# Kernel tuning notes

Hardware: AMD Instinct MI355X
Metric: run time of the kernel (lower is better)

The kernel has to match this reference:

```python
import jax, jax.numpy as jnp
import numpy as np

B, R, NM, H, P1, G1, RC1, LAT = 16384, 360, 200, 256, 512, 256, 256, 128


def _linear_params(k, out_f, in_f):
    s = 1.0 / np.sqrt(in_f)
    kw, kb = jax.random.split(k)
    W = jax.random.uniform(kw, (out_f, in_f), minval=-s, maxval=s, dtype=jnp.float32)
    b = jax.random.uniform(kb, (out_f,), minval=-s, maxval=s, dtype=jnp.float32)
    return W, b


def setup_inputs() -> dict:
    key = jax.random.key(0)
    ks = jax.random.split(key, 14)
    x_window = jax.random.normal(ks[0], (B, 3, R), dtype=jnp.float32)
    modes = jax.random.normal(ks[1], (R, NM), dtype=jnp.float32)
    mode_coeff = jax.random.normal(ks[2], (B, NM), dtype=jnp.float32)
    W1, b1 = _linear_params(ks[3], H, 3 * R)      # surrogate layer 1
    W2, b2 = _linear_params(ks[4], H, H)          # surrogate layer 2
    W3, b3 = _linear_params(ks[5], R, H)          # surrogate layer 3
    Wp1, bp1 = _linear_params(ks[6], P1, R * R)   # npi_proj
    Wp2, bp2 = _linear_params(ks[7], LAT, P1)
    Wg1, bg1 = _linear_params(ks[8], G1, NM)      # geo_proj
    Wg2, bg2 = _linear_params(ks[9], LAT, G1)
    Wr1, br1 = _linear_params(ks[10], RC1, LAT)   # recon
    Wr2, br2 = _linear_params(ks[11], R, RC1)
    return dict(x_window=x_window, modes=modes, mode_coeff=mode_coeff,
                W1=W1, b1=b1, W2=W2, b2=b2, W3=W3, b3=b3,
                Wp1=Wp1, bp1=bp1, Wp2=Wp2, bp2=bp2,
                Wg1=Wg1, bg1=bg1, Wg2=Wg2, bg2=bg2,
                Wr1=Wr1, br1=br1, Wr2=Wr2, br2=br2)


def reference(x_window, modes, mode_coeff,
              W1, b1, W2, b2, W3, b3,
              Wp1, bp1, Wp2, bp2,
              Wg1, bg1, Wg2, bg2,
              Wr1, br1, Wr2, br2):
    Bs = x_window.shape[0]
    Rr = W3.shape[0]
    # ---- NPI surrogate forward (needed for ReLU masks) ----
    z = x_window.reshape(Bs, 3 * Rr)                       # (B, 3R)
    h1 = z @ W1.T + b1                                     # (B, H)
    m1 = (h1 > 0).astype(z.dtype)
    h2 = (h1 * m1) @ W2.T + b2                             # (B, H)
    m2 = (h2 > 0).astype(z.dtype)
    # ---- EC: exact batch-mean Jacobian of the ReLU MLP w.r.t last timestep ----
    # mean_b [ W3 diag(m2_b) W2 diag(m1_b) W1_last ] = W3 @ (W2 * (m2^T m1 / B)) @ W1[:, -R:]
    G = (m2.T @ m1) / Bs                                   # (H, H)
    ec = W3 @ ((W2 * G) @ W1[:, -Rr:])                     # (R, R); row j = dy_j/dx
    ec = jax.lax.stop_gradient(ec)                         # create_graph=False in original
    # ---- projections ----
    ec_flat = ec.reshape(1, Rr * Rr)
    z_npi1 = jax.nn.relu(ec_flat @ Wp1.T + bp1) @ Wp2.T + bp2   # (1, LAT)
    z_npi = jnp.tile(z_npi1, (Bs, 1))                           # (B, LAT)
    z_geo = jax.nn.relu(mode_coeff @ Wg1.T + bg1) @ Wg2.T + bg2  # (B, LAT)
    zsum = z_npi + z_geo
    zn = zsum / jnp.maximum(jnp.linalg.norm(zsum, axis=-1, keepdims=True), 1e-12)
    recon = jax.nn.relu(zn @ Wr1.T + br1) @ Wr2.T + br2          # (B, R)
    return (z_npi, z_geo, zn, ec, recon)
```

## Files before the change

### kernel.cpp

```cpp
#include <hip/hip_runtime.h>

typedef __bf16 bf16x8 __attribute__((ext_vector_type(8)));
typedef __bf16 bf16x4 __attribute__((ext_vector_type(4)));
typedef float  f32x4  __attribute__((ext_vector_type(4)));

__device__ __forceinline__ f32x4 mfma_bf16(bf16x8 a, bf16x8 b, f32x4 c) {
  return __builtin_amdgcn_mfma_f32_16x16x32_bf16(a, b, c, 0, 0, 0);
}
__device__ __forceinline__ bf16x8 ldB(const __bf16* Bp, int kt, int NT, int nt,
                                      int lane) {
  return *reinterpret_cast<const bf16x8*>(Bp + (((size_t)kt * NT + nt) * 64 + lane) * 8);
}

__global__ void pack_all(const float* __restrict__ W1, const float* __restrict__ W2,
                         const float* __restrict__ Wg1, const float* __restrict__ Wg2,
                         const float* __restrict__ Wr1, const float* __restrict__ Wr2,
                         __bf16* __restrict__ W1p, __bf16* __restrict__ W2p,
                         __bf16* __restrict__ Wg1p, __bf16* __restrict__ Wg2p,
                         __bf16* __restrict__ Wr1p, __bf16* __restrict__ Wr2p) {
  int bx = blockIdx.x;
  const float* W; __bf16* out; int N, K, NT, local;
  if (bx < 544)      { W = W1;  out = W1p;  N = 256; K = 1080; NT = 16; local = bx; }
  else if (bx < 672) { W = W2;  out = W2p;  N = 256; K = 256;  NT = 16; local = bx - 544; }
  else if (bx < 784) { W = Wg1; out = Wg1p; N = 256; K = 200;  NT = 16; local = bx - 672; }
  else if (bx < 848) { W = Wg2; out = Wg2p; N = 128; K = 256;  NT = 8;  local = bx - 784; }
  else if (bx < 912) { W = Wr1; out = Wr1p; N = 256; K = 128;  NT = 16; local = bx - 848; }
  else               { W = Wr2; out = Wr2p; N = 360; K = 256;  NT = 24; local = bx - 912; }
  int nt = local % NT, kt = local / NT;
  int lane = threadIdx.x;
  int n = nt * 16 + (lane & 15);
  int k0 = kt * 32 + (lane >> 4) * 8;
  bf16x8 v;
#pragma unroll
  for (int e = 0; e < 8; ++e) {
    int k = k0 + e;
    float xv = (n < N && k < K) ? W[(size_t)n * K + k] : 0.f;
    v[e] = (__bf16)xv;
  }
  *reinterpret_cast<bf16x8*>(out + ((size_t)local * 64 + lane) * 8) = v;
}

__global__ __launch_bounds__(256) void h1h2_fused(
    const float* __restrict__ x, const __bf16* __restrict__ W1p,
    const float* __restrict__ b1, const __bf16* __restrict__ W2p,
    const float* __restrict__ b2, __bf16* __restrict__ m1b,
    __bf16* __restrict__ m2b) {
  __shared__ __bf16 Alds[32][40];
  __shared__ __bf16 h1s[32][264];
  int tid = threadIdx.x;
  int lane = tid & 63, wid = tid >> 6;
  int rowBase = blockIdx.x * 32;
  int sr = tid >> 3, sc = (tid & 7) * 4;
  const float* aSrc = x + (size_t)(rowBase + sr) * 1080;
  f32x4 acc[2][4] = {};
  float4 ld0 = *(const float4*)(aSrc + sc);
  float4 ld1 = *(const float4*)(aSrc + 32 + sc);
  for (int kt = 0; kt < 34; ++kt) {
    bf16x4 w4;
    w4[0] = (__bf16)ld0.x; w4[1] = (__bf16)ld0.y;
    w4[2] = (__bf16)ld0.z; w4[3] = (__bf16)ld0.w;
    *reinterpret_cast<bf16x4*>(&Alds[sr][sc]) = w4;
    __syncthreads();
    ld0 = ld1;
    if (kt + 2 < 34) {
      int gk = (kt + 2) * 32 + sc;
      ld1 = (gk < 1080) ? *(const float4*)(aSrc + gk) : make_float4(0.f, 0.f, 0.f, 0.f);
    }
    int arow = lane & 15, ak = (lane >> 4) * 8;
    bf16x8 a0 = *reinterpret_cast<const bf16x8*>(&Alds[arow][ak]);
    bf16x8 a1 = *reinterpret_cast<const bf16x8*>(&Alds[arow + 16][ak]);
#pragma unroll
    for (int n = 0; n < 4; ++n) {
      bf16x8 bv = ldB(W1p, kt, 16, wid * 4 + n, lane);
      acc[0][n] = mfma_bf16(a0, bv, acc[0][n]);
      acc[1][n] = mfma_bf16(a1, bv, acc[1][n]);
    }
    __syncthreads();
  }
  int q4 = (lane >> 4) * 4;
#pragma unroll
  for (int m = 0; m < 2; ++m)
#pragma unroll
    for (int n = 0; n < 4; ++n) {
      int col = wid * 64 + n * 16 + (lane & 15);
      float bb = b1[col];
#pragma unroll
      for (int j = 0; j < 4; ++j) {
        int rl = m * 16 + q4 + j;
        float h = acc[m][n][j] + bb;
        m1b[(size_t)(rowBase + rl) * 256 + col] = (__bf16)(h > 0.f ? 1.f : 0.f);
        h1s[rl][col] = (__bf16)fmaxf(h, 0.f);
      }
    }
  __syncthreads();
  f32x4 acc2[2][4] = {};
#pragma unroll
  for (int ks = 0; ks < 8; ++ks) {
    int arow = lane & 15, ak = ks * 32 + (lane >> 4) * 8;
    bf16x8 a0 = *reinterpret_cast<const bf16x8*>(&h1s[arow][ak]);
    bf16x8 a1 = *reinterpret_cast<const bf16x8*>(&h1s[arow + 16][ak]);
#pragma unroll
    for (int n = 0; n < 4; ++n) {
      bf16x8 bv = ldB(W2p, ks, 16, wid * 4 + n, lane);
      acc2[0][n] = mfma_bf16(a0, bv, acc2[0][n]);
      acc2[1][n] = mfma_bf16(a1, bv, acc2[1][n]);
    }
  }
#pragma unroll
  for (int m = 0; m < 2; ++m)
#pragma unroll
    for (int n = 0; n < 4; ++n) {
      int col = wid * 64 + n * 16 + (lane & 15);
      float bb = b2[col];
#pragma unroll
      for (int j = 0; j < 4; ++j) {
        int rl = m * 16 + q4 + j;
        float h = acc2[m][n][j] + bb;
        m2b[(size_t)(rowBase + rl) * 256 + col] = (__bf16)(h > 0.f ? 1.f : 0.f);
      }
    }
}

__global__ __launch_bounds__(256) void gemm_masks(
    const __bf16* __restrict__ m2, const __bf16* __restrict__ m1,
    float* __restrict__ Gpart) {
  __shared__ __bf16 Aft[64][40];
  __shared__ __bf16 Bft[64][40];
  int tid = threadIdx.x;
  int lane = tid & 63, wid = tid >> 6;
  int wr = wid >> 1, wc = wid & 1;
  int ibase = blockIdx.x * 64, jbase = blockIdx.y * 64;
  int b0 = blockIdx.z * 1024;
  int skk = tid >> 3, si0 = (tid & 7) * 8;
  f32x4 acc[2][2] = {};
  for (int c = 0; c < 32; ++c) {
    int bb = b0 + c * 32 + skk;
    bf16x8 va = *reinterpret_cast<const bf16x8*>(m2 + (size_t)bb * 256 + ibase + si0);
    bf16x8 vb = *reinterpret_cast<const bf16x8*>(m1 + (size_t)bb * 256 + jbase + si0);
#pragma unroll
    for (int e = 0; e < 8; ++e) {
      int r = si0 + e;
      int cc = skk ^ (((r >> 3) & 3) << 3);
      Aft[r][cc] = va[e];
      Bft[r][cc] = vb[e];
    }
    __syncthreads();
    int ar = wr * 32 + (lane & 15);
    int br = wc * 32 + (lane & 15);
    int k8 = (lane >> 4) * 8;
    bf16x8 a0 = *reinterpret_cast<const bf16x8*>(&Aft[ar][k8 ^ (((ar >> 3) & 3) << 3)]);
    bf16x8 a1 = *reinterpret_cast<const bf16x8*>(
        &Aft[ar + 16][k8 ^ ((((ar + 16) >> 3) & 3) << 3)]);
    bf16x8 bv0 = *reinterpret_cast<const bf16x8*>(&Bft[br][k8 ^ (((br >> 3) & 3) << 3)]);
    bf16x8 bv1 = *reinterpret_cast<const bf16x8*>(
        &Bft[br + 16][k8 ^ ((((br + 16) >> 3) & 3) << 3)]);
    acc[0][0] = mfma_bf16(a0, bv0, acc[0][0]);
    acc[0][1] = mfma_bf16(a0, bv1, acc[0][1]);
    acc[1][0] = mfma_bf16(a1, bv0, acc[1][0]);
    acc[1][1] = mfma_bf16(a1, bv1, acc[1][1]);
    __syncthreads();
  }
  float* dst = Gpart + (size_t)blockIdx.z * 65536;
  int q4 = (lane >> 4) * 4;
#pragma unroll
  for (int m = 0; m < 2; ++m)
#pragma unroll
    for (int n = 0; n < 2; ++n)
#pragma unroll
      for (int j = 0; j < 4; ++j) {
        int gi = ibase + wr * 32 + m * 16 + q4 + j;
        int gj = jbase + wc * 32 + n * 16 + (lane & 15);
        dst[(size_t)gi * 256 + gj] = acc[m][n][j];
      }
}

__global__ void reduce_G(const float* __restrict__ Gpart, float* __restrict__ G) {
  int i = blockIdx.x * 256 + threadIdx.x;
  float s = 0.f;
#pragma unroll
  for (int z = 0; z < 16; ++z) s += Gpart[(size_t)z * 65536 + i];
  G[i] = s * (1.f / 16384.f);
}

__global__ __launch_bounds__(256) void small_gemm(
    const float* __restrict__ A, const float* __restrict__ A2, int lda,
    const float* __restrict__ Bm, int ldb, float* __restrict__ C, int ldc,
    int M, int N, int K) {
  __shared__ float As[64][17];
  __shared__ float Bs[16][65];
  int t = threadIdx.x;
  int tx = t & 15, ty = t >> 4;
  int m0 = blockIdx.y * 64, n0 = blockIdx.x * 64;
  float acc[4][4] = {};
  for (int k0 = 0; k0 < K; k0 += 16) {
#pragma unroll
    for (int i = 0; i < 4; ++i) {
      int idx = t * 4 + i;
      int r = idx >> 4, kk = idx & 15;
      int gm = m0 + r, gk = k0 + kk;
      float v = (gm < M && gk < K) ? A[(size_t)gm * lda + gk] : 0.f;
      if (A2 && gm < M && gk < K) v *= A2[(size_t)gm * lda + gk];
      As[r][kk] = v;
      int kk2 = idx >> 6, cc = idx & 63;
      int gk2 = k0 + kk2, gn = n0 + cc;
      Bs[kk2][cc] = (gk2 < K && gn < N) ? Bm[(size_t)gk2 * ldb + gn] : 0.f;
    }
    __syncthreads();
#pragma unroll
    for (int kk = 0; kk < 16; ++kk)
#pragma unroll
      for (int i = 0; i < 4; ++i)
#pragma unroll
        for (int j = 0; j < 4; ++j)
          acc[i][j] += As[ty * 4 + i][kk] * Bs[kk][tx * 4 + j];
    __syncthreads();
  }
#pragma unroll
  for (int i = 0; i < 4; ++i)
#pragma unroll
    for (int j = 0; j < 4; ++j) {
      int gm = m0 + ty * 4 + i, gn = n0 + tx * 4 + j;
      if (gm < M && gn < N) C[(size_t)gm * ldc + gn] = acc[i][j];
    }
}

__global__ __launch_bounds__(512) void p_and_g1(
    const float* __restrict__ Wp1, const float* __restrict__ ec,
    const float* __restrict__ bp1, float* __restrict__ p,
    const float* __restrict__ mc, const __bf16* __restrict__ Wg1p,
    const float* __restrict__ bg1, __bf16* __restrict__ g1b) {
  __shared__ __bf16 Alds[64][40];
  __shared__ float redw[8];
  int t = threadIdx.x;
  if (blockIdx.x < 512) {
    int row = blockIdx.x;
    const float4* w = (const float4*)(Wp1 + (size_t)row * 129600);
    const float4* e = (const float4*)ec;
    float s = 0.f;
    for (int i = t; i < 32400; i += 512) {
      float4 a = w[i], b = e[i];
      s += a.x * b.x + a.y * b.y + a.z * b.z + a.w * b.w;
    }
    for (int o = 32; o; o >>= 1) s += __shfl_down(s, o);
    if ((t & 63) == 0) redw[t >> 6] = s;
    __syncthreads();
    if (t == 0) {
      float tot = 0.f;
#pragma unroll
      for (int i = 0; i < 8; ++i) tot += redw[i];
      p[row] = fmaxf(tot + bp1[row], 0.f);
    }
  } else {
    int lane = t & 63, wid = t >> 6;
    int wr = wid >> 2, wc = wid & 3;
    int rowBase = (blockIdx.x - 512) * 64;
    int sr = t >> 3, sc = (t & 7) * 4;
    const float* aSrc = mc + (size_t)(rowBase + sr) * 200;
    f32x4 acc[2][4] = {};
    for (int kt = 0; kt < 7; ++kt) {
      int gk = kt * 32 + sc;
      bf16x4 w4;
      if (gk < 200) {
        float4 v = *(const float4*)(aSrc + gk);
        w4[0] = (__bf16)v.x; w4[1] = (__bf16)v.y;
        w4[2] = (__bf16)v.z; w4[3] = (__bf16)v.w;
      } else {
        w4[0] = w4[1] = w4[2] = w4[3] = (__bf16)0.f;
      }
      *reinterpret_cast<bf16x4*>(&Alds[sr][sc]) = w4;
      __syncthreads();
      int arow = wr * 32 + (lane & 15), ak = (lane >> 4) * 8;
      bf16x8 a0 = *reinterpret_cast<const bf16x8*>(&Alds[arow][ak]);
      bf16x8 a1 = *reinterpret_cast<const bf16x8*>(&Alds[arow + 16][ak]);
#pragma unroll
      for (int n = 0; n < 4; ++n) {
        bf16x8 bv = ldB(Wg1p, kt, 16, wc * 4 + n, lane);
        acc[0][n] = mfma_bf16(a0, bv, acc[0][n]);
        acc[1][n] = mfma_bf16(a1, bv, acc[1][n]);
      }
      __syncthreads();
    }
    int q4 = (lane >> 4) * 4;
#pragma unroll
    for (int m = 0; m < 2; ++m)
#pragma unroll
      for (int n = 0; n < 4; ++n) {
        int col = wc * 64 + n * 16 + (lane & 15);
        float bb = bg1[col];
#pragma unroll
        for (int j = 0; j < 4; ++j) {
          int rl = wr * 32 + m * 16 + q4 + j;
          g1b[(size_t)(rowBase + rl) * 256 + col] =
              (__bf16)fmaxf(acc[m][n][j] + bb, 0.f);
        }
      }
  }
}

__global__ void gemv_z(const float* __restrict__ p, const float* __restrict__ Wp2,
                       const float* __restrict__ bp2, float* __restrict__ znpi1) {
  __shared__ float pl[512];
  int t = threadIdx.x;
  pl[t] = p[t];
  pl[t + 256] = p[t + 256];
  __syncthreads();
  if (t < 128) {
    float s = bp2[t];
    const float* w = Wp2 + (size_t)t * 512;
    for (int k = 0; k < 512; ++k) s += pl[k] * w[k];
    znpi1[t] = s;
  }
}

__global__ __launch_bounds__(512) void mega_tail(
    const __bf16* __restrict__ g1b, const __bf16* __restrict__ Wg2p,
    const float* __restrict__ bg2, const float* __restrict__ znpi1,
    const __bf16* __restrict__ Wr1p, const float* __restrict__ br1,
    const __bf16* __restrict__ Wr2p, const float* __restrict__ br2,
    float* __restrict__ o_zgeo, float* __restrict__ o_znpi,
    float* __restrict__ o_zn, float* __restrict__ o_rec) {
  __shared__ __align__(16) char smem[64 * 264 * 2 + 64 * 136 * 2];
  __bf16 (*Abig)[264] = (__bf16(*)[264])smem;
  __bf16 (*r1S)[264] = (__bf16(*)[264])smem;
  __bf16 (*znS)[136] = (__bf16(*)[136])(smem + 64 * 264 * 2);
  __shared__ float red[4][64];
  int tid = threadIdx.x;
  int lane = tid & 63, wid = tid >> 6;
  int wr = wid >> 2, wc = wid & 3;
  int rowBase = blockIdx.x * 64;
  int q4 = (lane >> 4) * 4;
  {
    int r = tid >> 3, c0 = (tid & 7) * 32;
    const __bf16* src = g1b + (size_t)(rowBase + r) * 256 + c0;
#pragma unroll
    for (int i = 0; i < 4; ++i)
      *reinterpret_cast<bf16x8*>(&Abig[r][c0 + i * 8]) =
          *reinterpret_cast<const bf16x8*>(src + i * 8);
  }
  __syncthreads();
  float zs[2][2][4];
  {
    f32x4 acc[2][2] = {};
#pragma unroll
    for (int ks = 0; ks < 8; ++ks) {
      int arow = wr * 32 + (lane & 15), ak = ks * 32 + (lane >> 4) * 8;
      bf16x8 a0 = *reinterpret_cast<const bf16x8*>(&Abig[arow][ak]);
      bf16x8 a1 = *reinterpret_cast<const bf16x8*>(&Abig[arow + 16][ak]);
#pragma unroll
      for (int n = 0; n < 2; ++n) {
        bf16x8 bv = ldB(Wg2p, ks, 8, wc * 2 + n, lane);
        acc[0][n] = mfma_bf16(a0, bv, acc[0][n]);
        acc[1][n] = mfma_bf16(a1, bv, acc[1][n]);
      }
    }
#pragma unroll
    for (int m = 0; m < 2; ++m)
#pragma unroll
      for (int n = 0; n < 2; ++n) {
        int col = wc * 32 + n * 16 + (lane & 15);
        float bb = bg2[col], zv = znpi1[col];
#pragma unroll
        for (int j = 0; j < 4; ++j) {
          int row = rowBase + wr * 32 + m * 16 + q4 + j;
          float zg = acc[m][n][j] + bb;
          o_zgeo[(size_t)row * 128 + col] = zg;
          o_znpi[(size_t)row * 128 + col] = zv;
          zs[m][n][j] = zg + zv;
        }
      }
#pragma unroll
    for (int m = 0; m < 2; ++m)
#pragma unroll
      for (int j = 0; j < 4; ++j) {
        float pp = zs[m][0][j] * zs[m][0][j] + zs[m][1][j] * zs[m][1][j];
        pp += __shfl_xor(pp, 1);
        pp += __shfl_xor(pp, 2);
        pp += __shfl_xor(pp, 4);
        pp += __shfl_xor(pp, 8);
        if ((lane & 15) == 0) red[wc][wr * 32 + m * 16 + q4 + j] = pp;
      }
    __syncthreads();
#pragma unroll
    for (int m = 0; m < 2; ++m)
#pragma unroll
      for (int n = 0; n < 2; ++n) {
        int col = wc * 32 + n * 16 + (lane & 15);
#pragma unroll
        for (int j = 0; j < 4; ++j) {
          int rl = wr * 32 + m * 16 + q4 + j;
          float ss = red[0][rl] + red[1][rl] + red[2][rl] + red[3][rl];
          float rn = 1.f / fmaxf(sqrtf(ss), 1e-12f);
          float z = zs[m][n][j] * rn;
          o_zn[(size_t)(rowBase + rl) * 128 + col] = z;
          znS[rl][col] = (__bf16)z;
        }
      }
  }
  __syncthreads();
  {
    f32x4 acc[2][4] = {};
#pragma unroll
    for (int ks = 0; ks < 4; ++ks) {
      int arow = wr * 32 + (lane & 15), ak = ks * 32 + (lane >> 4) * 8;
      bf16x8 a0 = *reinterpret_cast<const bf16x8*>(&znS[arow][ak]);
      bf16x8 a1 = *reinterpret_cast<const bf16x8*>(&znS[arow + 16][ak]);
#pragma unroll
      for (int n = 0; n < 4; ++n) {
        bf16x8 bv = ldB(Wr1p, ks, 16, wc * 4 + n, lane);
        acc[0][n] = mfma_bf16(a0, bv, acc[0][n]);
        acc[1][n] = mfma_bf16(a1, bv, acc[1][n]);
      }
    }
#pragma unroll
    for (int m = 0; m < 2; ++m)
#pragma unroll
      for (int n = 0; n < 4; ++n) {
        int col = wc * 64 + n * 16 + (lane & 15);
        float bb = br1[col];
#pragma unroll
        for (int j = 0; j < 4; ++j) {
          int rl = wr * 32 + m * 16 + q4 + j;
          r1S[rl][col] = (__bf16)fmaxf(acc[m][n][j] + bb, 0.f);
        }
      }
  }
  __syncthreads();
  {
    f32x4 acc[2][6] = {};
#pragma unroll
    for (int ks = 0; ks < 8; ++ks) {
      int arow = wr * 32 + (lane & 15), ak = ks * 32 + (lane >> 4) * 8;
      bf16x8 a0 = *reinterpret_cast<const bf16x8*>(&r1S[arow][ak]);
      bf16x8 a1 = *reinterpret_cast<const bf16x8*>(&r1S[arow + 16][ak]);
#pragma unroll
      for (int n = 0; n < 6; ++n) {
        bf16x8 bv = ldB(Wr2p, ks, 24, wc * 6 + n, lane);
        acc[0][n] = mfma_bf16(a0, bv, acc[0][n]);
        acc[1][n] = mfma_bf16(a1, bv, acc[1][n]);
      }
    }
#pragma unroll
    for (int m = 0; m < 2; ++m)
#pragma unroll
      for (int n = 0; n < 6; ++n) {
        int col = wc * 96 + n * 16 + (lane & 15);
        if (col < 360) {
          float bb = br2[col];
#pragma unroll
          for (int j = 0; j < 4; ++j) {
            int rl = wr * 32 + m * 16 + q4 + j;
            o_rec[(size_t)(rowBase + rl) * 360 + col] = acc[m][n][j] + bb;
          }
        }
      }
  }
}

extern "C" void kernel_launch(void* const* d_in, const int* in_sizes, int n_in,
                              void* d_out, int out_size, void* d_ws,
                              size_t ws_size, hipStream_t stream) {
  (void)in_sizes; (void)n_in; (void)out_size; (void)ws_size;
  const float* x   = (const float*)d_in[0];
  const float* mc  = (const float*)d_in[2];
  const float* W1  = (const float*)d_in[3];  const float* b1  = (const float*)d_in[4];
  const float* W2  = (const float*)d_in[5];  const float* b2  = (const float*)d_in[6];
  const float* W3  = (const float*)d_in[7];
  const float* Wp1 = (const float*)d_in[9];  const float* bp1 = (const float*)d_in[10];
  const float* Wp2 = (const float*)d_in[11]; const float* bp2 = (const float*)d_in[12];
  const float* Wg1 = (const float*)d_in[13]; const float* bg1 = (const float*)d_in[14];
  const float* Wg2 = (const float*)d_in[15]; const float* bg2 = (const float*)d_in[16];
  const float* Wr1 = (const float*)d_in[17]; const float* br1 = (const float*)d_in[18];
  const float* Wr2 = (const float*)d_in[19]; const float* br2 = (const float*)d_in[20];

  float* out = (float*)d_out;
  float* o_znpi = out;
  float* o_zgeo = out + 2097152;
  float* o_zn   = out + 4194304;
  float* o_ec   = out + 6291456;
  float* o_rec  = out + 6421056;

  char* ws = (char*)d_ws;
  __bf16* m1b   = (__bf16*)(ws + 0);
  __bf16* m2b   = (__bf16*)(ws + 8388608);
  __bf16* g1b   = (__bf16*)(ws + 16777216);
  float*  Gpart = (float*)(ws + 25165824);
  float*  G     = (float*)(ws + 29360128);
  float*  T     = (float*)(ws + 29622272);
  float*  p512  = (float*)(ws + 30015488);
  float*  znpi1 = (float*)(ws + 30017536);
  __bf16* W1p   = (__bf16*)(ws + 30018048);
  __bf16* W2p   = W1p  + (size_t)544 * 512;
  __bf16* Wg1p  = W2p  + (size_t)128 * 512;
  __bf16* Wg2p  = Wg1p + (size_t)112 * 512;
  __bf16* Wr1p  = Wg2p + (size_t)64 * 512;
  __bf16* Wr2p  = Wr1p + (size_t)64 * 512;

  pack_all<<<1104, 64, 0, stream>>>(W1, W2, Wg1, Wg2, Wr1, Wr2,
                                    W1p, W2p, Wg1p, Wg2p, Wr1p, Wr2p);
  h1h2_fused<<<512, 256, 0, stream>>>(x, W1p, b1, W2p, b2, m1b, m2b);
  gemm_masks<<<dim3(4, 4, 16), 256, 0, stream>>>(m2b, m1b, Gpart);
  reduce_G<<<256, 256, 0, stream>>>(Gpart, G);
  small_gemm<<<dim3(6, 4), 256, 0, stream>>>(W2, G, 256, W1 + 720, 1080, T, 384,
                                             256, 360, 256);
  small_gemm<<<dim3(6, 6), 256, 0, stream>>>(W3, nullptr, 256, T, 384, o_ec, 360,
                                             360, 360, 256);
  p_and_g1<<<768, 512, 0, stream>>>(Wp1, o_ec, bp1, p512, mc, Wg1p, bg1, g1b);
  gemv_z<<<1, 256, 0, stream>>>(p512, Wp2, bp2, znpi1);
  mega_tail<<<256, 512, 0, stream>>>(g1b, Wg2p, bg2, znpi1, Wr1p, br1, Wr2p, br2,
                                     o_zgeo, o_znpi, o_zn, o_rec);
}
```

Measured before the change: 261.8 us.

## Transpose mask layout, fuse G reduction via atomics, move geo layer 2 upstream

Writes the ReLU masks batch-transposed so the mask Gram GEMM reads MFMA operands straight from global memory without an LDS transpose or barriers. It accumulates G with atomics, zeroing it inside the pack kernel, which removes the partial buffer and the reduce kernel. It also fuses the second geo projection into p_and_g1 so the g1 intermediate never goes to memory, parallelizes the GEMV across 128 blocks, and doubles the K step in the first GEMM. The cost is float atomic contention, nondeterministic summation order, strided transposed mask stores, and extra LDS in p_and_g1 that may lower occupancy.

Result: faster. 245.9 us, median of 2 (-6.1%).

```diff
diff --git a/kernel.cpp b/kernel.cpp
--- a/kernel.cpp
+++ b/kernel.cpp
@@ -17,8 +17,17 @@
                          const float* __restrict__ Wr1, const float* __restrict__ Wr2,
                          __bf16* __restrict__ W1p, __bf16* __restrict__ W2p,
                          __bf16* __restrict__ Wg1p, __bf16* __restrict__ Wg2p,
-                         __bf16* __restrict__ Wr1p, __bf16* __restrict__ Wr2p) {
+                         __bf16* __restrict__ Wr1p, __bf16* __restrict__ Wr2p,
+                         float* __restrict__ G) {
   int bx = blockIdx.x;
+  int lane = threadIdx.x;
+  if (bx >= 1104) {
+    float4* g = (float4*)G;
+    int base = (bx - 1104) * 512 + lane;
+#pragma unroll
+    for (int i = 0; i < 8; ++i) g[base + i * 64] = make_float4(0.f, 0.f, 0.f, 0.f);
+    return;
+  }
   const float* W; __bf16* out; int N, K, NT, local;
   if (bx < 544)      { W = W1;  out = W1p;  N = 256; K = 1080; NT = 16; local = bx; }
   else if (bx < 672) { W = W2;  out = W2p;  N = 256; K = 256;  NT = 16; local = bx - 544; }
@@ -27,7 +36,6 @@
   else if (bx < 912) { W = Wr1; out = Wr1p; N = 256; K = 128;  NT = 16; local = bx - 848; }
   else               { W = Wr2; out = Wr2p; N = 360; K = 256;  NT = 24; local = bx - 912; }
   int nt = local % NT, kt = local / NT;
-  int lane = threadIdx.x;
   int n = nt * 16 + (lane & 15);
   int k0 = kt * 32 + (lane >> 4) * 8;
   bf16x8 v;
@@ -43,37 +51,50 @@
 __global__ __launch_bounds__(256) void h1h2_fused(
     const float* __restrict__ x, const __bf16* __restrict__ W1p,
     const float* __restrict__ b1, const __bf16* __restrict__ W2p,
-    const float* __restrict__ b2, __bf16* __restrict__ m1b,
-    __bf16* __restrict__ m2b) {
-  __shared__ __bf16 Alds[32][40];
+    const float* __restrict__ b2, __bf16* __restrict__ m1T,
+    __bf16* __restrict__ m2T) {
+  __shared__ __bf16 Alds[32][68];
   __shared__ __bf16 h1s[32][264];
   int tid = threadIdx.x;
   int lane = tid & 63, wid = tid >> 6;
   int rowBase = blockIdx.x * 32;
-  int sr = tid >> 3, sc = (tid & 7) * 4;
+  int sr = tid >> 3, sc = (tid & 7) * 8;
   const float* aSrc = x + (size_t)(rowBase + sr) * 1080;
   f32x4 acc[2][4] = {};
-  float4 ld0 = *(const float4*)(aSrc + sc);
-  float4 ld1 = *(const float4*)(aSrc + 32 + sc);
-  for (int kt = 0; kt < 34; ++kt) {
-    bf16x4 w4;
-    w4[0] = (__bf16)ld0.x; w4[1] = (__bf16)ld0.y;
-    w4[2] = (__bf16)ld0.z; w4[3] = (__bf16)ld0.w;
-    *reinterpret_cast<bf16x4*>(&Alds[sr][sc]) = w4;
-    __syncthreads();
-    ld0 = ld1;
-    if (kt + 2 < 34) {
-      int gk = (kt + 2) * 32 + sc;
-      ld1 = (gk < 1080) ? *(const float4*)(aSrc + gk) : make_float4(0.f, 0.f, 0.f, 0.f);
-    }
-    int arow = lane & 15, ak = (lane >> 4) * 8;
-    bf16x8 a0 = *reinterpret_cast<const bf16x8*>(&Alds[arow][ak]);
-    bf16x8 a1 = *reinterpret_cast<const bf16x8*>(&Alds[arow + 16][ak]);
-#pragma unroll
-    for (int n = 0; n < 4; ++n) {
-      bf16x8 bv = ldB(W1p, kt, 16, wid * 4 + n, lane);
-      acc[0][n] = mfma_bf16(a0, bv, acc[0][n]);
-      acc[1][n] = mfma_bf16(a1, bv, acc[1][n]);
+  float4 c0a, c0b, c1a, c1b;
+  auto LD = [&](int s, float4& a, float4& b) {
+    int gk = s * 64 + sc;
+    if (gk < 1080) {
+      a = *(const float4*)(aSrc + gk);
+      b = *(const float4*)(aSrc + gk + 4);
+    } else {
+      a = make_float4(0.f, 0.f, 0.f, 0.f);
+      b = a;
+    }
+  };
+  LD(0, c0a, c0b);
+  LD(1, c1a, c1b);
+  for (int s = 0; s < 17; ++s) {
+    bf16x8 w8;
+    w8[0] = (__bf16)c0a.x; w8[1] = (__bf16)c0a.y; w8[2] = (__bf16)c0a.z; w8[3] = (__bf16)c0a.w;
+    w8[4] = (__bf16)c0b.x; w8[5] = (__bf16)c0b.y; w8[6] = (__bf16)c0b.z; w8[7] = (__bf16)c0b.w;
+    *reinterpret_cast<bf16x8*>(&Alds[sr][sc]) = w8;
+    __syncthreads();
+    c0a = c1a; c0b = c1b;
+    if (s + 2 < 17) LD(s + 2, c1a, c1b);
+    int arow = lane & 15;
+#pragma unroll
+    for (int ks = 0; ks < 2; ++ks) {
+      int ak = ks * 32 + (lane >> 4) * 8;
+      bf16x8 a0 = *reinterpret_cast<const bf16x8*>(&Alds[arow][ak]);
+      bf16x8 a1 = *reinterpret_cast<const bf16x8*>(&Alds[arow + 16][ak]);
+      int kt = s * 2 + ks;
+#pragma unroll
+      for (int n = 0; n < 4; ++n) {
+        bf16x8 bv = ldB(W1p, kt, 16, wid * 4 + n, lane);
+        acc[0][n] = mfma_bf16(a0, bv, acc[0][n]);
+        acc[1][n] = mfma_bf16(a1, bv, acc[1][n]);
+      }
     }
     __syncthreads();
   }
@@ -88,7 +109,7 @@
       for (int j = 0; j < 4; ++j) {
         int rl = m * 16 + q4 + j;
         float h = acc[m][n][j] + bb;
-        m1b[(size_t)(rowBase + rl) * 256 + col] = (__bf16)(h > 0.f ? 1.f : 0.f);
+        m1T[(size_t)col * 16384 + rowBase + rl] = (__bf16)(h > 0.f ? 1.f : 0.f);
         h1s[rl][col] = (__bf16)fmaxf(h, 0.f);
       }
     }
@@ -116,51 +137,35 @@
       for (int j = 0; j < 4; ++j) {
         int rl = m * 16 + q4 + j;
         float h = acc2[m][n][j] + bb;
-        m2b[(size_t)(rowBase + rl) * 256 + col] = (__bf16)(h > 0.f ? 1.f : 0.f);
+        m2T[(size_t)col * 16384 + rowBase + rl] = (__bf16)(h > 0.f ? 1.f : 0.f);
       }
     }
 }
 
 __global__ __launch_bounds__(256) void gemm_masks(
-    const __bf16* __restrict__ m2, const __bf16* __restrict__ m1,
-    float* __restrict__ Gpart) {
-  __shared__ __bf16 Aft[64][40];
-  __shared__ __bf16 Bft[64][40];
+    const __bf16* __restrict__ m2T, const __bf16* __restrict__ m1T,
+    float* __restrict__ G) {
   int tid = threadIdx.x;
   int lane = tid & 63, wid = tid >> 6;
   int wr = wid >> 1, wc = wid & 1;
   int ibase = blockIdx.x * 64, jbase = blockIdx.y * 64;
-  int b0 = blockIdx.z * 1024;
-  int skk = tid >> 3, si0 = (tid & 7) * 8;
+  size_t b0 = (size_t)blockIdx.z * 1024 + (lane >> 4) * 8;
+  const __bf16* pa0 = m2T + (size_t)(ibase + wr * 32 + (lane & 15)) * 16384 + b0;
+  const __bf16* pa1 = pa0 + (size_t)16 * 16384;
+  const __bf16* pb0 = m1T + (size_t)(jbase + wc * 32 + (lane & 15)) * 16384 + b0;
+  const __bf16* pb1 = pb0 + (size_t)16 * 16384;
   f32x4 acc[2][2] = {};
+#pragma unroll 4
   for (int c = 0; c < 32; ++c) {
-    int bb = b0 + c * 32 + skk;
-    bf16x8 va = *reinterpret_cast<const bf16x8*>(m2 + (size_t)bb * 256 + ibase + si0);
-    bf16x8 vb = *reinterpret_cast<const bf16x8*>(m1 + (size_t)bb * 256 + jbase + si0);
-#pragma unroll
-    for (int e = 0; e < 8; ++e) {
-      int r = si0 + e;
-      int cc = skk ^ (((r >> 3) & 3) << 3);
-      Aft[r][cc] = va[e];
-      Bft[r][cc] = vb[e];
-    }
-    __syncthreads();
-    int ar = wr * 32 + (lane & 15);
-    int br = wc * 32 + (lane & 15);
-    int k8 = (lane >> 4) * 8;
-    bf16x8 a0 = *reinterpret_cast<const bf16x8*>(&Aft[ar][k8 ^ (((ar >> 3) & 3) << 3)]);
-    bf16x8 a1 = *reinterpret_cast<const bf16x8*>(
-        &Aft[ar + 16][k8 ^ ((((ar + 16) >> 3) & 3) << 3)]);
-    bf16x8 bv0 = *reinterpret_cast<const bf16x8*>(&Bft[br][k8 ^ (((br >> 3) & 3) << 3)]);
-    bf16x8 bv1 = *reinterpret_cast<const bf16x8*>(
-        &Bft[br + 16][k8 ^ ((((br + 16) >> 3) & 3) << 3)]);
+    bf16x8 a0 = *reinterpret_cast<const bf16x8*>(pa0 + c * 32);
+    bf16x8 a1 = *reinterpret_cast<const bf16x8*>(pa1 + c * 32);
+    bf16x8 bv0 = *reinterpret_cast<const bf16x8*>(pb0 + c * 32);
+    bf16x8 bv1 = *reinterpret_cast<const bf16x8*>(pb1 + c * 32);
     acc[0][0] = mfma_bf16(a0, bv0, acc[0][0]);
     acc[0][1] = mfma_bf16(a0, bv1, acc[0][1]);
     acc[1][0] = mfma_bf16(a1, bv0, acc[1][0]);
     acc[1][1] = mfma_bf16(a1, bv1, acc[1][1]);
-    __syncthreads();
-  }
-  float* dst = Gpart + (size_t)blockIdx.z * 65536;
+  }
   int q4 = (lane >> 4) * 4;
 #pragma unroll
   for (int m = 0; m < 2; ++m)
@@ -170,16 +175,8 @@
       for (int j = 0; j < 4; ++j) {
         int gi = ibase + wr * 32 + m * 16 + q4 + j;
         int gj = jbase + wc * 32 + n * 16 + (lane & 15);
-        dst[(size_t)gi * 256 + gj] = acc[m][n][j];
-      }
-}
-
-__global__ void reduce_G(const float* __restrict__ Gpart, float* __restrict__ G) {
-  int i = blockIdx.x * 256 + threadIdx.x;
-  float s = 0.f;
-#pragma unroll
-  for (int z = 0; z < 16; ++z) s += Gpart[(size_t)z * 65536 + i];
-  G[i] = s * (1.f / 16384.f);
+        atomicAdd(&G[(size_t)gi * 256 + gj], acc[m][n][j] * (1.f / 16384.f));
+      }
 }
 
 __global__ __launch_bounds__(256) void small_gemm(
@@ -228,8 +225,10 @@
     const float* __restrict__ Wp1, const float* __restrict__ ec,
     const float* __restrict__ bp1, float* __restrict__ p,
     const float* __restrict__ mc, const __bf16* __restrict__ Wg1p,
-    const float* __restrict__ bg1, __bf16* __restrict__ g1b) {
+    const float* __restrict__ bg1, const __bf16* __restrict__ Wg2p,
+    const float* __restrict__ bg2, float* __restrict__ o_zgeo) {
   __shared__ __bf16 Alds[64][40];
+  __shared__ __bf16 g1S[64][264];
   __shared__ float redw[8];
   int t = threadIdx.x;
   if (blockIdx.x < 512) {
@@ -256,6 +255,7 @@
     int rowBase = (blockIdx.x - 512) * 64;
     int sr = t >> 3, sc = (t & 7) * 4;
     const float* aSrc = mc + (size_t)(rowBase + sr) * 200;
+    int q4 = (lane >> 4) * 4;
     f32x4 acc[2][4] = {};
     for (int kt = 0; kt < 7; ++kt) {
       int gk = kt * 32 + sc;
@@ -280,7 +280,6 @@
       }
       __syncthreads();
     }
-    int q4 = (lane >> 4) * 4;
 #pragma unroll
     for (int m = 0; m < 2; ++m)
 #pragma unroll
@@ -290,8 +289,33 @@
 #pragma unroll
         for (int j = 0; j < 4; ++j) {
           int rl = wr * 32 + m * 16 + q4 + j;
-          g1b[(size_t)(rowBase + rl) * 256 + col] =
-              (__bf16)fmaxf(acc[m][n][j] + bb, 0.f);
+          g1S[rl][col] = (__bf16)fmaxf(acc[m][n][j] + bb, 0.f);
+        }
+      }
+    __syncthreads();
+    f32x4 acc2[2][2] = {};
+#pragma unroll
+    for (int ks = 0; ks < 8; ++ks) {
+      int arow = wr * 32 + (lane & 15), ak = ks * 32 + (lane >> 4) * 8;
+      bf16x8 a0 = *reinterpret_cast<const bf16x8*>(&g1S[arow][ak]);
+      bf16x8 a1 = *reinterpret_cast<const bf16x8*>(&g1S[arow + 16][ak]);
+#pragma unroll
+      for (int n = 0; n < 2; ++n) {
+        bf16x8 bv = ldB(Wg2p, ks, 8, wc * 2 + n, lane);
+        acc2[0][n] = mfma_bf16(a0, bv, acc2[0][n]);
+        acc2[1][n] = mfma_bf16(a1, bv, acc2[1][n]);
+      }
+    }
+#pragma unroll
+    for (int m = 0; m < 2; ++m)
+#pragma unroll
+      for (int n = 0; n < 2; ++n) {
+        int col = wc * 32 + n * 16 + (lane & 15);
+        float bb = bg2[col];
+#pragma unroll
+        for (int j = 0; j < 4; ++j) {
+          int row = rowBase + wr * 32 + m * 16 + q4 + j;
+          o_zgeo[(size_t)row * 128 + col] = acc2[m][n][j] + bb;
         }
       }
   }
@@ -299,102 +323,59 @@
 
 __global__ void gemv_z(const float* __restrict__ p, const float* __restrict__ Wp2,
                        const float* __restrict__ bp2, float* __restrict__ znpi1) {
-  __shared__ float pl[512];
+  int j = blockIdx.x;
   int t = threadIdx.x;
-  pl[t] = p[t];
-  pl[t + 256] = p[t + 256];
-  __syncthreads();
-  if (t < 128) {
-    float s = bp2[t];
-    const float* w = Wp2 + (size_t)t * 512;
-    for (int k = 0; k < 512; ++k) s += pl[k] * w[k];
-    znpi1[t] = s;
-  }
+  const float4* w = (const float4*)(Wp2 + (size_t)j * 512);
+  const float4* pp = (const float4*)p;
+  float4 a0 = w[t], b0 = pp[t];
+  float4 a1 = w[t + 64], b1 = pp[t + 64];
+  float s = a0.x * b0.x + a0.y * b0.y + a0.z * b0.z + a0.w * b0.w +
+            a1.x * b1.x + a1.y * b1.y + a1.z * b1.z + a1.w * b1.w;
+  for (int o = 32; o; o >>= 1) s += __shfl_down(s, o);
+  if (t == 0) znpi1[j] = s + bp2[j];
 }
 
 __global__ __launch_bounds__(512) void mega_tail(
-    const __bf16* __restrict__ g1b, const __bf16* __restrict__ Wg2p,
-    const float* __restrict__ bg2, const float* __restrict__ znpi1,
+    const float* __restrict__ zgeo, const float* __restrict__ znpi1,
     const __bf16* __restrict__ Wr1p, const float* __restrict__ br1,
     const __bf16* __restrict__ Wr2p, const float* __restrict__ br2,
-    float* __restrict__ o_zgeo, float* __restrict__ o_znpi,
-    float* __restrict__ o_zn, float* __restrict__ o_rec) {
-  __shared__ __align__(16) char smem[64 * 264 * 2 + 64 * 136 * 2];
-  __bf16 (*Abig)[264] = (__bf16(*)[264])smem;
-  __bf16 (*r1S)[264] = (__bf16(*)[264])smem;
-  __bf16 (*znS)[136] = (__bf16(*)[136])(smem + 64 * 264 * 2);
-  __shared__ float red[4][64];
+    float* __restrict__ o_znpi, float* __restrict__ o_zn,
+    float* __restrict__ o_rec) {
+  __shared__ __bf16 r1S[64][264];
+  __shared__ __bf16 znS[64][136];
+  __shared__ float znpiS[128];
   int tid = threadIdx.x;
   int lane = tid & 63, wid = tid >> 6;
   int wr = wid >> 2, wc = wid & 3;
   int rowBase = blockIdx.x * 64;
   int q4 = (lane >> 4) * 4;
+  if (tid < 128) znpiS[tid] = znpi1[tid];
+  __syncthreads();
   {
-    int r = tid >> 3, c0 = (tid & 7) * 32;
-    const __bf16* src = g1b + (size_t)(rowBase + r) * 256 + c0;
-#pragma unroll
-    for (int i = 0; i < 4; ++i)
-      *reinterpret_cast<bf16x8*>(&Abig[r][c0 + i * 8]) =
-          *reinterpret_cast<const bf16x8*>(src + i * 8);
-  }
-  __syncthreads();
-  float zs[2][2][4];
-  {
-    f32x4 acc[2][2] = {};
-#pragma unroll
-    for (int ks = 0; ks < 8; ++ks) {
-      int arow = wr * 32 + (lane & 15), ak = ks * 32 + (lane >> 4) * 8;
-      bf16x8 a0 = *reinterpret_cast<const bf16x8*>(&Abig[arow][ak]);
-      bf16x8 a1 = *reinterpret_cast<const bf16x8*>(&Abig[arow + 16][ak]);
-#pragma unroll
-      for (int n = 0; n < 2; ++n) {
-        bf16x8 bv = ldB(Wg2p, ks, 8, wc * 2 + n, lane);
-        acc[0][n] = mfma_bf16(a0, bv, acc[0][n]);
-        acc[1][n] = mfma_bf16(a1, bv, acc[1][n]);
-      }
-    }
-#pragma unroll
-    for (int m = 0; m < 2; ++m)
-#pragma unroll
-      for (int n = 0; n < 2; ++n) {
-        int col = wc * 32 + n * 16 + (lane & 15);
-        float bb = bg2[col], zv = znpi1[col];
-#pragma unroll
-        for (int j = 0; j < 4; ++j) {
-          int row = rowBase + wr * 32 + m * 16 + q4 + j;
-          float zg = acc[m][n][j] + bb;
-          o_zgeo[(size_t)row * 128 + col] = zg;
-          o_znpi[(size_t)row * 128 + col] = zv;
-          zs[m][n][j] = zg + zv;
-        }
-      }
-#pragma unroll
-    for (int m = 0; m < 2; ++m)
-#pragma unroll
-      for (int j = 0; j < 4; ++j) {
-        float pp = zs[m][0][j] * zs[m][0][j] + zs[m][1][j] * zs[m][1][j];
-        pp += __shfl_xor(pp, 1);
-        pp += __shfl_xor(pp, 2);
-        pp += __shfl_xor(pp, 4);
-        pp += __shfl_xor(pp, 8);
-        if ((lane & 15) == 0) red[wc][wr * 32 + m * 16 + q4 + j] = pp;
-      }
-    __syncthreads();
-#pragma unroll
-    for (int m = 0; m < 2; ++m)
-#pragma unroll
-      for (int n = 0; n < 2; ++n) {
-        int col = wc * 32 + n * 16 + (lane & 15);
-#pragma unroll
-        for (int j = 0; j < 4; ++j) {
-          int rl = wr * 32 + m * 16 + q4 + j;
-          float ss = red[0][rl] + red[1][rl] + red[2][rl] + red[3][rl];
-          float rn = 1.f / fmaxf(sqrtf(ss), 1e-12f);
-          float z = zs[m][n][j] * rn;
-          o_zn[(size_t)(rowBase + rl) * 128 + col] = z;
-          znS[rl][col] = (__bf16)z;
-        }
-      }
+    int rg = tid >> 5;
+    int c4 = (tid & 31) * 4;
+    float4 zp = make_float4(znpiS[c4], znpiS[c4 + 1], znpiS[c4 + 2], znpiS[c4 + 3]);
+#pragma unroll
+    for (int ri = 0; ri < 4; ++ri) {
+      int rl = rg + ri * 16;
+      int row = rowBase + rl;
+      float4 zg = *(const float4*)(zgeo + (size_t)row * 128 + c4);
+      float4 zs = make_float4(zg.x + zp.x, zg.y + zp.y, zg.z + zp.z, zg.w + zp.w);
+      *(float4*)(o_znpi + (size_t)row * 128 + c4) = zp;
+      float ss = zs.x * zs.x + zs.y * zs.y + zs.z * zs.z + zs.w * zs.w;
+      ss += __shfl_xor(ss, 1);
+      ss += __shfl_xor(ss, 2);
+      ss += __shfl_xor(ss, 4);
+      ss += __shfl_xor(ss, 8);
+      ss += __shfl_xor(ss, 16);
+      float rn = 1.f / fmaxf(sqrtf(ss), 1e-12f);
+      float4 zn = make_float4(zs.x * rn, zs.y * rn, zs.z * rn, zs.w * rn);
+      *(float4*)(o_zn + (size_t)row * 128 + c4) = zn;
+      bf16x4 znb;
+      znb[0] = (__bf16)zn.x; znb[1] = (__bf16)zn.y;
+      znb[2] = (__bf16)zn.z; znb[3] = (__bf16)zn.w;
+      *reinterpret_cast<bf16x4*>(&znS[rl][c4]) = znb;
+    }
   }
   __syncthreads();
   {
@@ -480,32 +461,30 @@
   float* o_rec  = out + 6421056;
 
   char* ws = (char*)d_ws;
-  __bf16* m1b   = (__bf16*)(ws + 0);
-  __bf16* m2b   = (__bf16*)(ws + 8388608);
-  __bf16* g1b   = (__bf16*)(ws + 16777216);
-  float*  Gpart = (float*)(ws + 25165824);
-  float*  G     = (float*)(ws + 29360128);
-  float*  T     = (float*)(ws + 29622272);
-  float*  p512  = (float*)(ws + 30015488);
-  float*  znpi1 = (float*)(ws + 30017536);
-  __bf16* W1p   = (__bf16*)(ws + 30018048);
+  __bf16* m1T   = (__bf16*)(ws + 0);
+  __bf16* m2T   = (__bf16*)(ws + 8388608);
+  float*  G     = (float*)(ws + 16777216);
+  float*  T     = (float*)(ws + 17039360);
+  float*  p512  = (float*)(ws + 17432576);
+  float*  znpi1 = (float*)(ws + 17434624);
+  __bf16* W1p   = (__bf16*)(ws + 17435648);
   __bf16* W2p   = W1p  + (size_t)544 * 512;
   __bf16* Wg1p  = W2p  + (size_t)128 * 512;
   __bf16* Wg2p  = Wg1p + (size_t)112 * 512;
   __bf16* Wr1p  = Wg2p + (size_t)64 * 512;
   __bf16* Wr2p  = Wr1p + (size_t)64 * 512;
 
-  pack_all<<<1104, 64, 0, stream>>>(W1, W2, Wg1, Wg2, Wr1, Wr2,
-                                    W1p, W2p, Wg1p, Wg2p, Wr1p, Wr2p);
-  h1h2_fused<<<512, 256, 0, stream>>>(x, W1p, b1, W2p, b2, m1b, m2b);
-  gemm_masks<<<dim3(4, 4, 16), 256, 0, stream>>>(m2b, m1b, Gpart);
-  reduce_G<<<256, 256, 0, stream>>>(Gpart, G);
+  pack_all<<<1136, 64, 0, stream>>>(W1, W2, Wg1, Wg2, Wr1, Wr2,
+                                    W1p, W2p, Wg1p, Wg2p, Wr1p, Wr2p, G);
+  h1h2_fused<<<512, 256, 0, stream>>>(x, W1p, b1, W2p, b2, m1T, m2T);
+  gemm_masks<<<dim3(4, 4, 16), 256, 0, stream>>>(m2T, m1T, G);
   small_gemm<<<dim3(6, 4), 256, 0, stream>>>(W2, G, 256, W1 + 720, 1080, T, 384,
                                              256, 360, 256);
   small_gemm<<<dim3(6, 6), 256, 0, stream>>>(W3, nullptr, 256, T, 384, o_ec, 360,
                                              360, 360, 256);
-  p_and_g1<<<768, 512, 0, stream>>>(Wp1, o_ec, bp1, p512, mc, Wg1p, bg1, g1b);
-  gemv_z<<<1, 256, 0, stream>>>(p512, Wp2, bp2, znpi1);
-  mega_tail<<<256, 512, 0, stream>>>(g1b, Wg2p, bg2, znpi1, Wr1p, br1, Wr2p, br2,
-                                     o_zgeo, o_znpi, o_zn, o_rec);
-}
+  p_and_g1<<<768, 512, 0, stream>>>(Wp1, o_ec, bp1, p512, mc, Wg1p, bg1,
+                                    Wg2p, bg2, o_zgeo);
+  gemv_z<<<128, 64, 0, stream>>>(p512, Wp2, bp2, znpi1);
+  mega_tail<<<256, 512, 0, stream>>>(o_zgeo, znpi1, Wr1p, br1, Wr2p, br2,
+                                     o_znpi, o_zn, o_rec);
+}
```
